# Performance work log

Hardware: AMD Instinct MI355X
Metric: run time of the kernel (lower is better)

Reference implementation:

```python
import jax, jax.numpy as jnp
import numpy as np

D_MODEL = 512
D_DOWN = 64          # q and k each have this width; downsample outputs 2*D_DOWN
DIST_BINS = 64
ANGLE_BINS = 36
D_HID = DIST_BINS + ANGLE_BINS  # MLP hidden and output width (100)


def setup_inputs() -> dict:
    key = jax.random.key(0)
    ks = jax.random.split(key, 7)
    B, N = 2, 512
    s_down = 1.0 / np.sqrt(D_MODEL)
    s1 = 1.0 / np.sqrt(2 * D_DOWN)
    s2 = 1.0 / np.sqrt(D_HID)
    return {
        "x": jax.random.normal(ks[0], (B, N, D_MODEL), dtype=jnp.float32),
        "W_down": jax.random.uniform(ks[1], (D_MODEL, 2 * D_DOWN), jnp.float32, -s_down, s_down),
        "b_down": jax.random.uniform(ks[2], (2 * D_DOWN,), jnp.float32, -s_down, s_down),
        "W1": jax.random.uniform(ks[3], (2 * D_DOWN, D_HID), jnp.float32, -s1, s1),
        "b1": jax.random.uniform(ks[4], (D_HID,), jnp.float32, -s1, s1),
        "W2": jax.random.uniform(ks[5], (D_HID, D_HID), jnp.float32, -s2, s2),
        "b2": jax.random.uniform(ks[6], (D_HID,), jnp.float32, -s2, s2),
    }


def reference(x, W_down, b_down, W1, b1, W2, b2):
    # downsample: [B,N,d_model] -> [B,N,2*d_down], split into q,k of d_down each
    qk = x @ W_down + b_down
    q, k = jnp.split(qk, 2, axis=-1)              # each [B,N,d_down]
    q_i = q[:, :, None, :]                        # [B,N,1,d]
    k_j = k[:, None, :, :]                        # [B,1,N,d]
    pw = jnp.concatenate([q_i * k_j, k_j - q_i], axis=-1)  # [B,N,N,2*d_down]
    h = jax.nn.silu(pw @ W1 + b1)                 # [B,N,N,D_HID]
    out = h @ W2 + b2                             # [B,N,N,D_HID]
    distogram = out[..., :DIST_BINS]
    anglogram = out[..., DIST_BINS:]
    return (distogram, anglogram)
```

## Files before the change

### kernel.cpp

```cpp
#include <hip/hip_runtime.h>
#include <hip/hip_bf16.h>
#include <cstdint>

#define NBATCH 2
#define NSEQ   512
#define DHID   100

typedef __bf16 bf16x8 __attribute__((ext_vector_type(8)));
typedef __bf16 bf16x4 __attribute__((ext_vector_type(4)));
typedef float  f32x4  __attribute__((ext_vector_type(4)));

__global__ __launch_bounds__(128)
void proj_kernel(const float* __restrict__ x, const float* __restrict__ Wd,
                 const float* __restrict__ bd, float* __restrict__ qk)
{
    __shared__ float xs[512];
    const int row = blockIdx.x;
    const int tid = threadIdx.x;
    const float* xr = x + row * 512;
    #pragma unroll
    for (int e = 0; e < 4; e++) xs[tid + 128 * e] = xr[tid + 128 * e];
    __syncthreads();
    float a0 = 0.f, a1 = 0.f, a2 = 0.f, a3 = 0.f;
    const float* wp = Wd + tid;
    #pragma unroll 4
    for (int e = 0; e < 512; e += 4) {
        a0 = fmaf(xs[e],     wp[(e)     * 128], a0);
        a1 = fmaf(xs[e + 1], wp[(e + 1) * 128], a1);
        a2 = fmaf(xs[e + 2], wp[(e + 2) * 128], a2);
        a3 = fmaf(xs[e + 3], wp[(e + 3) * 128], a3);
    }
    qk[row * 128 + tid] = bd[tid] + ((a0 + a1) + (a2 + a3));
}


#define LDS_W2T  28672
#define LDS_H    57344
#define LDS_TOT  122880

__global__ __launch_bounds__(512, 2)
void pair_mlp_kernel(const float* __restrict__ qk,
                     const float* __restrict__ W1, const float* __restrict__ b1,
                     const float* __restrict__ W2, const float* __restrict__ b2,
                     float* __restrict__ dist, float* __restrict__ ang)
{
    extern __shared__ char smem[];
    const int tid  = threadIdx.x;
    const int w    = tid >> 6;
    const int lane = tid & 63;
    const int l16  = lane & 15;
    const int g    = lane >> 4;
    const int swz  = (l16 & 7) << 4;

    for (int idx = tid; idx < LDS_TOT / 4; idx += 512)
        ((float*)smem)[idx] = 0.f;
    __syncthreads();

    for (int idx = tid; idx < 100 * 128; idx += 512) {
        int n = idx >> 7, k = idx & 127;
        int byte = n * 256 + ((2 * k) ^ ((n & 7) << 4));
        *(__bf16*)(smem + byte) = (__bf16)W1[k * DHID + n];
    }
    for (int idx = tid; idx < 100 * 100; idx += 512) {
        int n = idx / 100, k = idx % 100;
        int byte = LDS_W2T + n * 256 + ((2 * k) ^ ((n & 7) << 4));
        *(__bf16*)(smem + byte) = (__bf16)W2[k * DHID + n];
    }
    __syncthreads();

    f32x4 b1v[7], b2v[7];
    #pragma unroll
    for (int nt = 0; nt < 7; nt++) {
        int n0 = nt * 16 + g * 4;
        if (n0 + 3 < DHID) { b1v[nt] = *(const f32x4*)(b1 + n0); b2v[nt] = *(const f32x4*)(b2 + n0); }
        else               { b1v[nt] = (f32x4){0,0,0,0};         b2v[nt] = (f32x4){0,0,0,0}; }
    }

    char* hb = smem + LDS_H + w * 8192;
    const int TILES = NBATCH * (NSEQ / 8) * (NSEQ / 32);

    for (int t = blockIdx.x; t < TILES; t += gridDim.x) {
        int tmp = t;
        const int jb = tmp & 15;  tmp >>= 4;
        const int ib = tmp & 63;  tmp >>= 6;
        const int bi = tmp;
        const int i  = ib * 8 + w;
        const int j0 = jb * 32;

        const float* qrow = qk + (size_t)(bi * NSEQ + i) * 128;
        f32x4 qa0 = *(const f32x4*)(qrow + g * 8);
        f32x4 qa1 = *(const f32x4*)(qrow + g * 8 + 4);
        f32x4 qb0 = *(const f32x4*)(qrow + 32 + g * 8);
        f32x4 qb1 = *(const f32x4*)(qrow + 32 + g * 8 + 4);

        bf16x8 af[2][4];
        #pragma unroll
        for (int s = 0; s < 2; s++) {
            const float* krow = qk + (size_t)(bi * NSEQ + j0 + s * 16 + l16) * 128 + 64;
            f32x4 ka0 = *(const f32x4*)(krow + g * 8);
            f32x4 ka1 = *(const f32x4*)(krow + g * 8 + 4);
            f32x4 kb0 = *(const f32x4*)(krow + 32 + g * 8);
            f32x4 kb1 = *(const f32x4*)(krow + 32 + g * 8 + 4);
            #pragma unroll
            for (int j = 0; j < 4; j++) {
                af[s][0][j]     = (__bf16)(qa0[j] * ka0[j]);
                af[s][0][j + 4] = (__bf16)(qa1[j] * ka1[j]);
                af[s][1][j]     = (__bf16)(qb0[j] * kb0[j]);
                af[s][1][j + 4] = (__bf16)(qb1[j] * kb1[j]);
                af[s][2][j]     = (__bf16)(ka0[j] - qa0[j]);
                af[s][2][j + 4] = (__bf16)(ka1[j] - qa1[j]);
                af[s][3][j]     = (__bf16)(kb0[j] - qb0[j]);
                af[s][3][j + 4] = (__bf16)(kb1[j] - qb1[j]);
            }
        }

        f32x4 acc1[2][7];
        #pragma unroll
        for (int nt = 0; nt < 7; nt++) { acc1[0][nt] = b1v[nt]; acc1[1][nt] = b1v[nt]; }
        #pragma unroll
        for (int nt = 0; nt < 7; nt++) {
            const int rbase = (nt * 16 + l16) * 256;
            #pragma unroll
            for (int ks = 0; ks < 4; ks++) {
                bf16x8 wf = *(const bf16x8*)(smem + rbase + ((64 * ks + 16 * g) ^ swz));
                acc1[0][nt] = __builtin_amdgcn_mfma_f32_16x16x32_bf16(wf, af[0][ks], acc1[0][nt], 0, 0, 0);
                acc1[1][nt] = __builtin_amdgcn_mfma_f32_16x16x32_bf16(wf, af[1][ks], acc1[1][nt], 0, 0, 0);
            }
        }

        #pragma unroll
        for (int s = 0; s < 2; s++) {
            char* hrow = hb + (s * 16 + l16) * 256;
            #pragma unroll
            for (int nt = 0; nt < 7; nt++) {
                bf16x4 hv;
                #pragma unroll
                for (int r = 0; r < 4; r++) {
                    float z = acc1[s][nt][r];
                    float v = z * __builtin_amdgcn_rcpf(1.f + __expf(-z));
                    if (nt == 6 && g > 0) v = 0.f;
                    hv[r] = (__bf16)v;
                }
                *(bf16x4*)(hrow + ((nt * 32 + g * 8) ^ swz)) = hv;
            }
        }

        f32x4 acc2[2][7];
        #pragma unroll
        for (int nt = 0; nt < 7; nt++) { acc2[0][nt] = b2v[nt]; acc2[1][nt] = b2v[nt]; }
        #pragma unroll
        for (int ks = 0; ks < 4; ks++) {
            bf16x8 ah[2];
            #pragma unroll
            for (int s = 0; s < 2; s++)
                ah[s] = *(const bf16x8*)(hb + (s * 16 + l16) * 256 + ((ks * 64 + g * 16) ^ swz));
            #pragma unroll
            for (int nt = 0; nt < 7; nt++) {
                bf16x8 wf = *(const bf16x8*)(smem + LDS_W2T + (nt * 16 + l16) * 256 + ((ks * 64 + 16 * g) ^ swz));
                acc2[0][nt] = __builtin_amdgcn_mfma_f32_16x16x32_bf16(wf, ah[0], acc2[0][nt], 0, 0, 0);
                acc2[1][nt] = __builtin_amdgcn_mfma_f32_16x16x32_bf16(wf, ah[1], acc2[1][nt], 0, 0, 0);
            }
        }

        const size_t rowbase = (size_t)(bi * NSEQ + i) * NSEQ + j0;
        #pragma unroll
        for (int s = 0; s < 2; s++) {
            size_t prow = rowbase + s * 16 + l16;
            float* dp = dist + prow * 64;
            float* ap = ang  + prow * 36;
            #pragma unroll
            for (int nt = 0; nt < 4; nt++)
                *(f32x4*)(dp + nt * 16 + g * 4) = acc2[s][nt];
            *(f32x4*)(ap + g * 4)      = acc2[s][4];
            *(f32x4*)(ap + 16 + g * 4) = acc2[s][5];
            if (g == 0) *(f32x4*)(ap + 32) = acc2[s][6];
        }
    }
}

extern "C" void kernel_launch(void* const* d_in, const int* in_sizes, int n_in,
                              void* d_out, int out_size, void* d_ws, size_t ws_size,
                              hipStream_t stream) {
    const float* x  = (const float*)d_in[0];
    const float* Wd = (const float*)d_in[1];
    const float* bd = (const float*)d_in[2];
    const float* W1 = (const float*)d_in[3];
    const float* b1 = (const float*)d_in[4];
    const float* W2 = (const float*)d_in[5];
    const float* b2 = (const float*)d_in[6];

    float* dist = (float*)d_out;
    float* ang  = dist + (size_t)NBATCH * NSEQ * NSEQ * 64;
    float* qk   = (float*)d_ws;

    (void)hipFuncSetAttribute(reinterpret_cast<const void*>(&pair_mlp_kernel),
                              hipFuncAttributeMaxDynamicSharedMemorySize, LDS_TOT);

    proj_kernel<<<NBATCH * NSEQ, 128, 0, stream>>>(x, Wd, bd, qk);
    pair_mlp_kernel<<<256, 512, LDS_TOT, stream>>>(qk, W1, b1, W2, b2, dist, ang);
}
```

Before: 250.8 us.

## Keep hidden activations in registers and feed layer-2 via 16x16x16 MFMA

Removes the per-wave LDS staging buffer for the hidden activations. The accumulator layout of the first MFMA is reused directly as the B operand of 16x16x16 bf16 MFMAs, with W2 repacked in LDS so its rows match that register layout. Biases move to LDS instead of registers, and the unused final k-chunk is skipped. The smaller LDS footprint lets the launch bound allow 4 blocks per CU, and the grid doubles to 512 blocks. In exchange the second GEMM runs twice as many smaller MFMA instructions, and register pressure may limit the intended occupancy.

```diff
diff --git a/kernel.cpp b/kernel.cpp
--- a/kernel.cpp
+++ b/kernel.cpp
@@ -9,6 +9,19 @@
 typedef __bf16 bf16x8 __attribute__((ext_vector_type(8)));
 typedef __bf16 bf16x4 __attribute__((ext_vector_type(4)));
 typedef float  f32x4  __attribute__((ext_vector_type(4)));
+typedef short  short4v __attribute__((ext_vector_type(4)));
+
+static __device__ __forceinline__ f32x4 mfma16(bf16x4 a, bf16x4 b, f32x4 c) {
+#if __has_builtin(__builtin_amdgcn_mfma_f32_16x16x16bf16_1k)
+    return __builtin_amdgcn_mfma_f32_16x16x16bf16_1k(
+        __builtin_bit_cast(short4v, a), __builtin_bit_cast(short4v, b), c, 0, 0, 0);
+#else
+    f32x4 d = c;
+    asm("v_mfma_f32_16x16x16_bf16 %0, %1, %2, %0\n\ts_nop 7"
+        : "+v"(d) : "v"(a), "v"(b));
+    return d;
+#endif
+}
 
 __global__ __launch_bounds__(128)
 void proj_kernel(const float* __restrict__ x, const float* __restrict__ Wd,
@@ -34,17 +47,18 @@
 }
 
 
-#define LDS_W2T  28672
-#define LDS_H    57344
-#define LDS_TOT  122880
-
-__global__ __launch_bounds__(512, 2)
+#define LDS_W2P  28672
+#define LDS_B1   57344
+#define LDS_B2   57792
+#define LDS_TOT  58240
+
+__global__ __launch_bounds__(512, 4)
 void pair_mlp_kernel(const float* __restrict__ qk,
                      const float* __restrict__ W1, const float* __restrict__ b1,
                      const float* __restrict__ W2, const float* __restrict__ b2,
                      float* __restrict__ dist, float* __restrict__ ang)
 {
-    extern __shared__ char smem[];
+    __shared__ char smem[LDS_TOT];
     const int tid  = threadIdx.x;
     const int w    = tid >> 6;
     const int lane = tid & 63;
@@ -63,20 +77,18 @@
     }
     for (int idx = tid; idx < 100 * 100; idx += 512) {
         int n = idx / 100, k = idx % 100;
-        int byte = LDS_W2T + n * 256 + ((2 * k) ^ ((n & 7) << 4));
+        int ks = k >> 4, p = ks >> 1, half = ks & 1, gg = (k >> 2) & 3, j = k & 3;
+        int bin = p * 64 + gg * 16 + half * 8 + 2 * j;
+        int byte = LDS_W2P + n * 256 + (bin ^ ((n & 7) << 4));
         *(__bf16*)(smem + byte) = (__bf16)W2[k * DHID + n];
     }
+    if (tid < DHID) {
+        ((float*)(smem + LDS_B1))[tid] = b1[tid];
+        ((float*)(smem + LDS_B2))[tid] = b2[tid];
+    }
     __syncthreads();
 
-    f32x4 b1v[7], b2v[7];
-    #pragma unroll
-    for (int nt = 0; nt < 7; nt++) {
-        int n0 = nt * 16 + g * 4;
-        if (n0 + 3 < DHID) { b1v[nt] = *(const f32x4*)(b1 + n0); b2v[nt] = *(const f32x4*)(b2 + n0); }
-        else               { b1v[nt] = (f32x4){0,0,0,0};         b2v[nt] = (f32x4){0,0,0,0}; }
-    }
-
-    char* hb = smem + LDS_H + w * 8192;
+    const int bia = (g * 4) * 4;
     const int TILES = NBATCH * (NSEQ / 8) * (NSEQ / 32);
 
     for (int t = blockIdx.x; t < TILES; t += gridDim.x) {
@@ -116,7 +128,10 @@
 
         f32x4 acc1[2][7];
         #pragma unroll
-        for (int nt = 0; nt < 7; nt++) { acc1[0][nt] = b1v[nt]; acc1[1][nt] = b1v[nt]; }
+        for (int nt = 0; nt < 7; nt++) {
+            f32x4 bv = *(const f32x4*)(smem + LDS_B1 + nt * 64 + bia);
+            acc1[0][nt] = bv; acc1[1][nt] = bv;
+        }
         #pragma unroll
         for (int nt = 0; nt < 7; nt++) {
             const int rbase = (nt * 16 + l16) * 256;
@@ -128,37 +143,37 @@
             }
         }
 
-        #pragma unroll
-        for (int s = 0; s < 2; s++) {
-            char* hrow = hb + (s * 16 + l16) * 256;
-            #pragma unroll
-            for (int nt = 0; nt < 7; nt++) {
-                bf16x4 hv;
+        bf16x4 hf[2][7];
+        #pragma unroll
+        for (int s = 0; s < 2; s++)
+            #pragma unroll
+            for (int nt = 0; nt < 7; nt++)
                 #pragma unroll
                 for (int r = 0; r < 4; r++) {
                     float z = acc1[s][nt][r];
-                    float v = z * __builtin_amdgcn_rcpf(1.f + __expf(-z));
-                    if (nt == 6 && g > 0) v = 0.f;
-                    hv[r] = (__bf16)v;
+                    hf[s][nt][r] = (__bf16)(z * __builtin_amdgcn_rcpf(1.f + __expf(-z)));
                 }
-                *(bf16x4*)(hrow + ((nt * 32 + g * 8) ^ swz)) = hv;
-            }
-        }
 
         f32x4 acc2[2][7];
         #pragma unroll
-        for (int nt = 0; nt < 7; nt++) { acc2[0][nt] = b2v[nt]; acc2[1][nt] = b2v[nt]; }
-        #pragma unroll
-        for (int ks = 0; ks < 4; ks++) {
-            bf16x8 ah[2];
-            #pragma unroll
-            for (int s = 0; s < 2; s++)
-                ah[s] = *(const bf16x8*)(hb + (s * 16 + l16) * 256 + ((ks * 64 + g * 16) ^ swz));
-            #pragma unroll
-            for (int nt = 0; nt < 7; nt++) {
-                bf16x8 wf = *(const bf16x8*)(smem + LDS_W2T + (nt * 16 + l16) * 256 + ((ks * 64 + 16 * g) ^ swz));
-                acc2[0][nt] = __builtin_amdgcn_mfma_f32_16x16x32_bf16(wf, ah[0], acc2[0][nt], 0, 0, 0);
-                acc2[1][nt] = __builtin_amdgcn_mfma_f32_16x16x32_bf16(wf, ah[1], acc2[1][nt], 0, 0, 0);
+        for (int nt = 0; nt < 7; nt++) {
+            f32x4 bv = *(const f32x4*)(smem + LDS_B2 + nt * 64 + bia);
+            acc2[0][nt] = bv; acc2[1][nt] = bv;
+        }
+        #pragma unroll
+        for (int nt = 0; nt < 7; nt++) {
+            const char* rbase = smem + LDS_W2P + (nt * 16 + l16) * 256;
+            #pragma unroll
+            for (int p = 0; p < 4; p++) {
+                bf16x8 wv = *(const bf16x8*)(rbase + ((p * 64 + 16 * g) ^ swz));
+                bf16x4 wlo = __builtin_shufflevector(wv, wv, 0, 1, 2, 3);
+                bf16x4 whi = __builtin_shufflevector(wv, wv, 4, 5, 6, 7);
+                acc2[0][nt] = mfma16(wlo, hf[0][2 * p], acc2[0][nt]);
+                acc2[1][nt] = mfma16(wlo, hf[1][2 * p], acc2[1][nt]);
+                if (p < 3) {
+                    acc2[0][nt] = mfma16(whi, hf[0][2 * p + 1], acc2[0][nt]);
+                    acc2[1][nt] = mfma16(whi, hf[1][2 * p + 1], acc2[1][nt]);
+                }
             }
         }
 
@@ -193,9 +208,6 @@
     float* ang  = dist + (size_t)NBATCH * NSEQ * NSEQ * 64;
     float* qk   = (float*)d_ws;
 
-    (void)hipFuncSetAttribute(reinterpret_cast<const void*>(&pair_mlp_kernel),
-                              hipFuncAttributeMaxDynamicSharedMemorySize, LDS_TOT);
-
     proj_kernel<<<NBATCH * NSEQ, 128, 0, stream>>>(x, Wd, bd, qk);
-    pair_mlp_kernel<<<256, 512, LDS_TOT, stream>>>(qk, W1, b1, W2, b2, dist, ang);
-}
+    pair_mlp_kernel<<<512, 512, 0, stream>>>(qk, W1, b1, W2, b2, dist, ang);
+}
```

Measured after the change: 538.9 us. 115% more time.
